# Optimization experiments

Measured on AMD Instinct MI355X. Metric: run time of the kernel, lower is better.

Reference implementation:

```python
import jax, jax.numpy as jnp
import numpy as np

N_HEAD = 16
ROPE_BASE = 10000.0


def _rotate_half(x):
    # interleaved rotate: (-x2, x1) pairs, matching torch stack+flatten
    x1 = x[..., ::2]
    x2 = x[..., 1::2]
    return jnp.stack((-x2, x1), axis=-1).reshape(x.shape)


def setup_inputs() -> dict:
    key = jax.random.key(0)
    ks = jax.random.split(key, 5)
    B, S, C = 4, 2048, 1024
    sc = 1.0 / np.sqrt(C)
    return {
        "x": jax.random.normal(ks[0], (B, S, C), jnp.float32),
        "W_qkv": jax.random.normal(ks[1], (C, 3 * C), jnp.float32) * sc,
        "b_qkv": jax.random.normal(ks[2], (3 * C,), jnp.float32) * 0.02,
        "W_proj": jax.random.normal(ks[3], (C, C), jnp.float32) * sc,
        "b_proj": jax.random.normal(ks[4], (C,), jnp.float32) * 0.02,
    }


def reference(x, W_qkv, b_qkv, W_proj, b_proj):
    B, S, C = x.shape
    H = N_HEAD
    D = C // H

    qkv = x @ W_qkv + b_qkv                       # [B,S,3C]
    q, k, v = jnp.split(qkv, 3, axis=-1)
    q = q.reshape(B, S, H, D).transpose(0, 2, 1, 3)  # [B,H,S,D]
    k = k.reshape(B, S, H, D).transpose(0, 2, 1, 3)
    v = v.reshape(B, S, H, D).transpose(0, 2, 1, 3)

    # RoPE cache (offset=0), faithful to source: emb = cat(freqs, freqs)
    inv_freq = 1.0 / (ROPE_BASE ** (jnp.arange(0, D, 2, dtype=jnp.float32) / D))
    pos = jnp.arange(S, dtype=jnp.float32)
    freqs = jnp.outer(pos, inv_freq)              # [S, D/2]
    emb = jnp.concatenate((freqs, freqs), axis=-1)  # [S, D]
    cos = jnp.cos(emb)[None, None, :, :]
    sin = jnp.sin(emb)[None, None, :, :]

    q = q * cos + _rotate_half(q) * sin
    k = k * cos + _rotate_half(k) * sin

    scale = 1.0 / jnp.sqrt(jnp.asarray(D, x.dtype))
    scores = jnp.einsum("bhqd,bhkd->bhqk", q, k) * scale  # [B,H,S,S]
    causal = jnp.tril(jnp.ones((S, S), dtype=bool))
    scores = jnp.where(causal[None, None], scores, jnp.asarray(-jnp.inf, x.dtype))
    att = jax.nn.softmax(scores, axis=-1)
    out = jnp.einsum("bhqk,bhkd->bhqd", att, v)    # [B,H,S,D]

    out = out.transpose(0, 2, 1, 3).reshape(B, S, C)
    out = out @ W_proj + b_proj                    # dropout=0 (eval)
    return out
```

## Files before the change

### kernel.cpp

```cpp
#include <hip/hip_runtime.h>
#include <hip/hip_bf16.h>
#include <math.h>

#define B_ 4
#define S_ 2048
#define C_ 1024
#define H_ 16
#define D_ 64
#define M_ (B_*S_)
#define NQKV (3*C_)
#define KDIM C_

typedef float f32x4 __attribute__((ext_vector_type(4)));
typedef float f32x16 __attribute__((ext_vector_type(16)));
typedef short bf16x8 __attribute__((ext_vector_type(8)));

static __device__ __forceinline__ ushort f2bf(float f){
    __hip_bfloat16 h = __float2bfloat16(f);
    union { __hip_bfloat16 b; ushort u; } v; v.b = h;
    return v.u;
}

static __device__ __forceinline__ void gload16(const ushort* g, ushort* l){
    __builtin_amdgcn_global_load_lds((__attribute__((address_space(1))) void*)g,
                                     (__attribute__((address_space(3))) void*)l,
                                     16, 0, 0);
}

__global__ void k_conv(const float* __restrict__ in, ushort* __restrict__ out, int n4){
    int i = blockIdx.x*blockDim.x + threadIdx.x;
    if (i < n4){
        float4 v = *(const float4*)(in + i*4);
        ushort4 o;
        o.x = f2bf(v.x); o.y = f2bf(v.y); o.z = f2bf(v.z); o.w = f2bf(v.w);
        *(ushort4*)(out + i*4) = o;
    }
}

__global__ void k_transpose(const float* __restrict__ in, ushort* __restrict__ out,
                            int R, int Ccol){
    __shared__ float tile[32][33];
    int c0 = blockIdx.x*32, r0 = blockIdx.y*32;
    int tx = threadIdx.x, ty = threadIdx.y;
    for (int j = ty; j < 32; j += 8)
        tile[j][tx] = in[(r0 + j)*Ccol + c0 + tx];
    __syncthreads();
    for (int j = ty; j < 32; j += 8)
        out[(size_t)(c0 + tx)*R + r0 + j] = f2bf(tile[j][tx]);
}

__global__ void k_cs_tab(unsigned* __restrict__ csT){
    int t = blockIdx.x*blockDim.x + threadIdx.x;
    if (t >= D_*S_) return;
    int d = t >> 11, pos = t & 2047;
    float invf = powf(10000.0f, -(float)(d & 31) / 32.0f);
    float ang = (float)pos * invf;
    csT[t] = (unsigned)f2bf(cosf(ang)) | ((unsigned)f2bf(sinf(ang)) << 16);
}

__launch_bounds__(512, 4)
__global__ void k_qkv(const ushort* __restrict__ xb, const ushort* __restrict__ wt,
                      const float* __restrict__ bqkv, const unsigned* __restrict__ csT,
                      ushort* __restrict__ qb, ushort* __restrict__ kb, ushort* __restrict__ vT){
    __shared__ __align__(16) ushort As[2][256][32];
    __shared__ __align__(16) ushort Bs[2][128][32];
    int bid = blockIdx.x;
    int lin = (bid & 7)*96 + (bid >> 3);
    int bx = lin % 24, by = lin / 24;
    int M0 = by*256, N0 = bx*128;
    int tid = threadIdx.x;
    int wid = tid >> 6, lane = tid & 63;
    int wm = wid >> 1, wn = wid & 1;
    int lrow = lane & 15, lk = lane >> 4;
    int swu = (lrow >> 1) & 3;

    int scol = (((lane & 3) ^ ((lane >> 3) & 3))) * 8;
    const ushort* gA0 = &xb[(size_t)(M0 + wid*16 + (lane >> 2))*KDIM + scol];
    const ushort* gA1 = gA0 + (size_t)128*KDIM;
    const ushort* gB0 = &wt[(size_t)(N0 + wid*16 + (lane >> 2))*KDIM + scol];

    f32x4 acc[4][4] = {};
    gload16(gA0, &As[0][wid*16][0]);
    gload16(gA1, &As[0][128 + wid*16][0]);
    gload16(gB0, &Bs[0][wid*16][0]);

    int cur = 0;
    for (int k0 = 0; k0 < KDIM; k0 += 32){
        int nk = k0 + 32;
        if (nk < KDIM){
            gload16(gA0 + nk, &As[cur^1][wid*16][0]);
            gload16(gA1 + nk, &As[cur^1][128 + wid*16][0]);
            gload16(gB0 + nk, &Bs[cur^1][wid*16][0]);
            __builtin_amdgcn_sched_barrier(0);
            asm volatile("s_waitcnt vmcnt(3)" ::: "memory");
        } else {
            asm volatile("s_waitcnt vmcnt(0)" ::: "memory");
        }
        __builtin_amdgcn_s_barrier();
        __builtin_amdgcn_sched_barrier(0);
        bf16x8 a[4], b[4];
#pragma unroll
        for (int mi = 0; mi < 4; mi++)
            a[mi] = *(const bf16x8*)(&As[cur][wm*64 + mi*16 + lrow][(lk ^ swu)*8]);
#pragma unroll
        for (int ni = 0; ni < 4; ni++)
            b[ni] = *(const bf16x8*)(&Bs[cur][wn*64 + ni*16 + lrow][(lk ^ swu)*8]);
#pragma unroll
        for (int mi = 0; mi < 4; mi++)
#pragma unroll
            for (int ni = 0; ni < 4; ni++)
                acc[mi][ni] = __builtin_amdgcn_mfma_f32_16x16x32_bf16(a[mi], b[ni], acc[mi][ni], 0, 0, 0);
        __builtin_amdgcn_sched_barrier(0);
        asm volatile("s_waitcnt lgkmcnt(0)" ::: "memory");
        __builtin_amdgcn_s_barrier();
        cur ^= 1;
    }
#pragma unroll
    for (int mi = 0; mi < 4; mi++)
#pragma unroll
    for (int ni = 0; ni < 4; ni++){
        int gn = N0 + wn*64 + ni*16 + lrow;
        float bias = bqkv[gn];
        int which = gn >> 10;
        int cn = gn & 1023;
        int h = cn >> 6, d = cn & 63;
        int gm0 = M0 + wm*64 + mi*16 + lk*4;
        int bb = gm0 >> 11, pos0 = gm0 & 2047;
        if (which == 2){
            ushort4 o = { f2bf(acc[mi][ni][0] + bias), f2bf(acc[mi][ni][1] + bias),
                          f2bf(acc[mi][ni][2] + bias), f2bf(acc[mi][ni][3] + bias) };
            *(ushort4*)(&vT[(((size_t)(bb*H_ + h))*D_ + d)*S_ + pos0]) = o;
        } else {
            uint4 cs4 = *(const uint4*)(&csT[d*2048 + pos0]);
            unsigned csa[4] = { cs4.x, cs4.y, cs4.z, cs4.w };
#pragma unroll
            for (int rr = 0; rr < 4; rr++){
                float val = acc[mi][ni][rr] + bias;
                float rot = __shfl_xor(val, 1);
                unsigned cs = csa[rr];
                float c = __uint_as_float(cs << 16);
                float s = __uint_as_float(cs & 0xffff0000u);
                float o = val*c + ((d & 1) ? rot : -rot)*s;
                if (which == 0) o *= 0.18033688f;
                int out_idx = (((bb*H_ + h)*S_) + pos0 + rr)*D_ + d;
                ((which == 0) ? qb : kb)[out_idx] = f2bf(o);
            }
        }
    }
}

__launch_bounds__(512, 4)
__global__ void k_proj(const ushort* __restrict__ ab, const ushort* __restrict__ wt,
                       const float* __restrict__ bias, float* __restrict__ out){
    __shared__ __align__(16) ushort As[2][256][32];
    __shared__ __align__(16) ushort Bs[2][128][32];
    int bid = blockIdx.x;
    int lin = (bid & 7)*32 + (bid >> 3);
    int bx = lin & 7, by = lin >> 3;
    int M0 = by*256, N0 = bx*128;
    int tid = threadIdx.x;
    int wid = tid >> 6, lane = tid & 63;
    int wm = wid >> 1, wn = wid & 1;
    int lrow = lane & 15, lk = lane >> 4;
    int swu = (lrow >> 1) & 3;

    int scol = (((lane & 3) ^ ((lane >> 3) & 3))) * 8;
    const ushort* gA0 = &ab[(size_t)(M0 + wid*16 + (lane >> 2))*KDIM + scol];
    const ushort* gA1 = gA0 + (size_t)128*KDIM;
    const ushort* gB0 = &wt[(size_t)(N0 + wid*16 + (lane >> 2))*KDIM + scol];

    f32x4 acc[4][4] = {};
    gload16(gA0, &As[0][wid*16][0]);
    gload16(gA1, &As[0][128 + wid*16][0]);
    gload16(gB0, &Bs[0][wid*16][0]);

    int cur = 0;
    for (int k0 = 0; k0 < KDIM; k0 += 32){
        int nk = k0 + 32;
        if (nk < KDIM){
            gload16(gA0 + nk, &As[cur^1][wid*16][0]);
            gload16(gA1 + nk, &As[cur^1][128 + wid*16][0]);
            gload16(gB0 + nk, &Bs[cur^1][wid*16][0]);
            __builtin_amdgcn_sched_barrier(0);
            asm volatile("s_waitcnt vmcnt(3)" ::: "memory");
        } else {
            asm volatile("s_waitcnt vmcnt(0)" ::: "memory");
        }
        __builtin_amdgcn_s_barrier();
        __builtin_amdgcn_sched_barrier(0);
        bf16x8 a[4], b[4];
#pragma unroll
        for (int mi = 0; mi < 4; mi++)
            a[mi] = *(const bf16x8*)(&As[cur][wm*64 + mi*16 + lrow][(lk ^ swu)*8]);
#pragma unroll
        for (int ni = 0; ni < 4; ni++)
            b[ni] = *(const bf16x8*)(&Bs[cur][wn*64 + ni*16 + lrow][(lk ^ swu)*8]);
#pragma unroll
        for (int mi = 0; mi < 4; mi++)
#pragma unroll
            for (int ni = 0; ni < 4; ni++)
                acc[mi][ni] = __builtin_amdgcn_mfma_f32_16x16x32_bf16(a[mi], b[ni], acc[mi][ni], 0, 0, 0);
        __builtin_amdgcn_sched_barrier(0);
        asm volatile("s_waitcnt lgkmcnt(0)" ::: "memory");
        __builtin_amdgcn_s_barrier();
        cur ^= 1;
    }
#pragma unroll
    for (int mi = 0; mi < 4; mi++)
#pragma unroll
    for (int ni = 0; ni < 4; ni++){
        int gn = N0 + wn*64 + ni*16 + lrow;
        float bv = bias[gn];
#pragma unroll
        for (int rr = 0; rr < 4; rr++){
            int gm = M0 + wm*64 + mi*16 + lk*4 + rr;
            out[(size_t)gm*C_ + gn] = acc[mi][ni][rr] + bv;
        }
    }
}

__launch_bounds__(256, 3)
__global__ void k_attn(const ushort* __restrict__ qb, const ushort* __restrict__ kb,
                       const ushort* __restrict__ vT, ushort* __restrict__ ob){
    __shared__ __align__(16) ushort Ks[64][64];
    __shared__ __align__(16) ushort Vs[64][64];
    int bh = blockIdx.x;
    int qt = (gridDim.y - 1) - blockIdx.y;
    int bb = bh >> 4, h = bh & 15;
    int tid = threadIdx.x, wid = tid >> 6, lane = tid & 63;
    int lq = lane & 31, hi = lane >> 5;
    const ushort* qp = qb + (size_t)bh*S_*D_;
    const ushort* kp = kb + (size_t)bh*S_*D_;
    const ushort* vp = vT + (size_t)bh*D_*S_;
    int qw = qt*128 + wid*32;
    int qrow = qw + lq;
    int swz = lq & 7;

    bf16x8 fq[4];
#pragma unroll
    for (int c = 0; c < 4; c++)
        fq[c] = *(const bf16x8*)(&qp[qrow*D_ + c*16 + hi*8]);

    f32x16 acc0 = {}, acc1 = {};
    float m = -1e30f, l = 0.0f;

    int tr = tid >> 3, tcu = tid & 7;
    int twu = (tcu ^ (tr & 7)) * 8;
    int tc = tcu * 8;

    int4 ra = *(const int4*)(&kp[tr*D_ + tc]);
    int4 rb = *(const int4*)(&kp[(tr+32)*D_ + tc]);
    int4 rc = *(const int4*)(&vp[(size_t)tr*S_ + tc]);
    int4 rd = *(const int4*)(&vp[(size_t)(tr+32)*S_ + tc]);

    int nit = 2*qt + 2;
    for (int it = 0; it < nit; ++it){
        int j0 = it*64;
        *(int4*)(&Ks[tr][twu])    = ra;
        *(int4*)(&Ks[tr+32][twu]) = rb;
        *(int4*)(&Vs[tr][twu])    = rc;
        *(int4*)(&Vs[tr+32][twu]) = rd;
        __syncthreads();
        if (it + 1 < nit){
            int j1 = j0 + 64;
            ra = *(const int4*)(&kp[(j1+tr)*D_ + tc]);
            rb = *(const int4*)(&kp[(j1+tr+32)*D_ + tc]);
            rc = *(const int4*)(&vp[(size_t)tr*S_ + j1 + tc]);
            rd = *(const int4*)(&vp[(size_t)(tr+32)*S_ + j1 + tc]);
        }
        int rel = qw - j0;
        if (rel >= 0){
            bool diag0 = (rel == 0);
            bool have1 = (rel >= 32);
            bool diag1 = (rel == 32);
            f32x16 z0 = {}, z1 = {};
#pragma unroll
            for (int c = 0; c < 4; c++){
                bf16x8 kf = *(const bf16x8*)(&Ks[lq][((2*c + hi) ^ swz)*8]);
                z0 = __builtin_amdgcn_mfma_f32_32x32x16_bf16(kf, fq[c], z0, 0, 0, 0);
            }
            if (have1){
#pragma unroll
                for (int c = 0; c < 4; c++){
                    bf16x8 kf = *(const bf16x8*)(&Ks[32 + lq][((2*c + hi) ^ swz)*8]);
                    z1 = __builtin_amdgcn_mfma_f32_32x32x16_bf16(kf, fq[c], z1, 0, 0, 0);
                }
            }
            if (diag0){
#pragma unroll
                for (int r = 0; r < 16; r++)
                    if (((r & 3) + 8*(r >> 2) + 4*hi) > lq) z0[r] = -1e30f;
            }
            if (diag1){
#pragma unroll
                for (int r = 0; r < 16; r++)
                    if (((r & 3) + 8*(r >> 2) + 4*hi) > lq) z1[r] = -1e30f;
            }
            float tmax = z0[0];
#pragma unroll
            for (int r = 1; r < 16; r++) tmax = fmaxf(tmax, z0[r]);
            if (have1){
#pragma unroll
                for (int r = 0; r < 16; r++) tmax = fmaxf(tmax, z1[r]);
            }
            tmax = fmaxf(tmax, __shfl_xor(tmax, 32));
            if (__any(tmax > m)){
                float newm = fmaxf(m, tmax);
                float resc = exp2f(m - newm);
                m = newm; l *= resc;
#pragma unroll
                for (int r = 0; r < 16; r++){ acc0[r] *= resc; acc1[r] *= resc; }
            }
            float rsum = 0.0f;
#pragma unroll
            for (int r = 0; r < 16; r++){ z0[r] = exp2f(z0[r] - m); rsum += z0[r]; }
            if (have1){
#pragma unroll
                for (int r = 0; r < 16; r++){ z1[r] = exp2f(z1[r] - m); rsum += z1[r]; }
            }
            rsum += __shfl_xor(rsum, 32);
            l += rsum;

#define PV_SUB(zz, r0_, su, t) do {                                              \
    unsigned w0, w1, w2, w3;                                                     \
    asm("v_cvt_pk_bf16_f32 %0, %1, %2" : "=v"(w0) : "v"(zz[r0_+0]), "v"(zz[r0_+1])); \
    asm("v_cvt_pk_bf16_f32 %0, %1, %2" : "=v"(w1) : "v"(zz[r0_+2]), "v"(zz[r0_+3])); \
    asm("v_cvt_pk_bf16_f32 %0, %1, %2" : "=v"(w2) : "v"(zz[r0_+4]), "v"(zz[r0_+5])); \
    asm("v_cvt_pk_bf16_f32 %0, %1, %2" : "=v"(w3) : "v"(zz[r0_+6]), "v"(zz[r0_+7])); \
    auto s02 = __builtin_amdgcn_permlane32_swap(w0, w2, false, false);            \
    auto s13 = __builtin_amdgcn_permlane32_swap(w1, w3, false, false);            \
    union { unsigned u[4]; bf16x8 v; } pf;                                       \
    pf.u[0] = s02[0]; pf.u[1] = s13[0]; pf.u[2] = s02[1]; pf.u[3] = s13[1];      \
    bf16x8 vf0 = *(const bf16x8*)(&Vs[lq][(((su)*4 + (t)*2 + hi) ^ swz)*8]);     \
    acc0 = __builtin_amdgcn_mfma_f32_32x32x16_bf16(vf0, pf.v, acc0, 0, 0, 0);    \
    bf16x8 vf1 = *(const bf16x8*)(&Vs[32 + lq][(((su)*4 + (t)*2 + hi) ^ swz)*8]);\
    acc1 = __builtin_amdgcn_mfma_f32_32x32x16_bf16(vf1, pf.v, acc1, 0, 0, 0);    \
} while(0)

            PV_SUB(z0, 0, 0, 0);
            PV_SUB(z0, 8, 0, 1);
            if (have1){
                PV_SUB(z1, 0, 1, 0);
                PV_SUB(z1, 8, 1, 1);
            }
#undef PV_SUB
        }
        __syncthreads();
    }
    float rl = 1.0f / l;
#pragma unroll
    for (int rg = 0; rg < 4; rg++){
        ushort4 o0 = { f2bf(acc0[rg*4+0]*rl), f2bf(acc0[rg*4+1]*rl),
                       f2bf(acc0[rg*4+2]*rl), f2bf(acc0[rg*4+3]*rl) };
        *(ushort4*)(&ob[((size_t)(bb*S_ + qrow))*C_ + h*D_ + rg*8 + hi*4]) = o0;
        ushort4 o1 = { f2bf(acc1[rg*4+0]*rl), f2bf(acc1[rg*4+1]*rl),
                       f2bf(acc1[rg*4+2]*rl), f2bf(acc1[rg*4+3]*rl) };
        *(ushort4*)(&ob[((size_t)(bb*S_ + qrow))*C_ + h*D_ + 32 + rg*8 + hi*4]) = o1;
    }
}

extern "C" void kernel_launch(void* const* d_in, const int* in_sizes, int n_in,
                              void* d_out, int out_size, void* d_ws, size_t ws_size,
                              hipStream_t stream) {
    const float* x     = (const float*)d_in[0];
    const float* Wqkv  = (const float*)d_in[1];
    const float* bqkv  = (const float*)d_in[2];
    const float* Wproj = (const float*)d_in[3];
    const float* bproj = (const float*)d_in[4];
    float* out = (float*)d_out;

    char* ws = (char*)d_ws;
    ushort*   xb   = (ushort*)(ws);
    ushort*   wqt  = (ushort*)(ws + (16u<<20));
    ushort*   wpt  = (ushort*)(ws + (22u<<20));
    unsigned* csT  = (unsigned*)(ws + (24u<<20));
    ushort*   qbuf = (ushort*)(ws + (25u<<20));
    ushort*   kbuf = (ushort*)(ws + (41u<<20));
    ushort*   vbuf = (ushort*)(ws + (57u<<20));
    ushort*   obuf = (ushort*)(ws + (73u<<20));

    k_conv<<<(M_*KDIM/4 + 255)/256, 256, 0, stream>>>(x, xb, M_*KDIM/4);
    dim3 tb(32, 8);
    k_transpose<<<dim3(NQKV/32, KDIM/32), tb, 0, stream>>>(Wqkv, wqt, KDIM, NQKV);
    k_transpose<<<dim3(C_/32, KDIM/32), tb, 0, stream>>>(Wproj, wpt, KDIM, C_);
    k_cs_tab<<<(D_*S_ + 255)/256, 256, 0, stream>>>(csT);

    k_qkv<<<768, 512, 0, stream>>>(xb, wqt, bqkv, csT, qbuf, kbuf, vbuf);
    k_attn<<<dim3(B_*H_, S_/128), 256, 0, stream>>>(qbuf, kbuf, vbuf, obuf);
    k_proj<<<256, 512, 0, stream>>>(obuf, wpt, bproj, out);
}
```

Baseline: 200.7 us.

## Merge prep kernels into one launch, simplify GEMM sync, add attention setprio

Folds the four preprocessing kernels (x bf16 conversion, two weight transposes, RoPE cos/sin table) into one kernel that picks its job by block-index range. This cuts launch count and tail gaps between small kernels. The QKV and projection GEMM loops drop the hand-placed vmcnt/lgkmcnt waits and sched barriers in favour of plain __syncthreads, with one sync after the prologue. That may change how well the next-tile loads overlap with the MFMAs. The attention kernel raises wave priority around the QK and PV MFMA blocks so matrix work is issued ahead of other waves.

```diff
diff --git a/kernel.cpp b/kernel.cpp
--- a/kernel.cpp
+++ b/kernel.cpp
@@ -27,35 +27,44 @@
                                      16, 0, 0);
 }
 
-__global__ void k_conv(const float* __restrict__ in, ushort* __restrict__ out, int n4){
-    int i = blockIdx.x*blockDim.x + threadIdx.x;
-    if (i < n4){
-        float4 v = *(const float4*)(in + i*4);
-        ushort4 o;
-        o.x = f2bf(v.x); o.y = f2bf(v.y); o.z = f2bf(v.z); o.w = f2bf(v.w);
-        *(ushort4*)(out + i*4) = o;
-    }
-}
-
-__global__ void k_transpose(const float* __restrict__ in, ushort* __restrict__ out,
-                            int R, int Ccol){
+__global__ void k_prep(const float* __restrict__ x, const float* __restrict__ Wqkv,
+                       const float* __restrict__ Wproj,
+                       ushort* __restrict__ xb, ushort* __restrict__ wqt,
+                       ushort* __restrict__ wpt, unsigned* __restrict__ csT){
     __shared__ float tile[32][33];
-    int c0 = blockIdx.x*32, r0 = blockIdx.y*32;
-    int tx = threadIdx.x, ty = threadIdx.y;
-    for (int j = ty; j < 32; j += 8)
-        tile[j][tx] = in[(r0 + j)*Ccol + c0 + tx];
-    __syncthreads();
-    for (int j = ty; j < 32; j += 8)
-        out[(size_t)(c0 + tx)*R + r0 + j] = f2bf(tile[j][tx]);
-}
-
-__global__ void k_cs_tab(unsigned* __restrict__ csT){
-    int t = blockIdx.x*blockDim.x + threadIdx.x;
-    if (t >= D_*S_) return;
-    int d = t >> 11, pos = t & 2047;
-    float invf = powf(10000.0f, -(float)(d & 31) / 32.0f);
-    float ang = (float)pos * invf;
-    csT[t] = (unsigned)f2bf(cosf(ang)) | ((unsigned)f2bf(sinf(ang)) << 16);
+    int blk = blockIdx.x, tid = threadIdx.x;
+    if (blk < 2048){
+        const int n4 = M_*KDIM/4;
+        for (int i = blk*256 + tid; i < n4; i += 2048*256){
+            float4 v = *(const float4*)(x + (size_t)i*4);
+            ushort4 o = { f2bf(v.x), f2bf(v.y), f2bf(v.z), f2bf(v.w) };
+            *(ushort4*)(xb + (size_t)i*4) = o;
+        }
+    } else if (blk < 5120){
+        int t = blk - 2048;
+        int c0 = (t % 96)*32, r0 = (t / 96)*32;
+        int tx = tid & 31, ty = tid >> 5;
+        for (int j = ty; j < 32; j += 8)
+            tile[j][tx] = Wqkv[(size_t)(r0 + j)*NQKV + c0 + tx];
+        __syncthreads();
+        for (int j = ty; j < 32; j += 8)
+            wqt[(size_t)(c0 + tx)*KDIM + r0 + j] = f2bf(tile[j][tx]);
+    } else if (blk < 6144){
+        int t = blk - 5120;
+        int c0 = (t & 31)*32, r0 = (t >> 5)*32;
+        int tx = tid & 31, ty = tid >> 5;
+        for (int j = ty; j < 32; j += 8)
+            tile[j][tx] = Wproj[(size_t)(r0 + j)*C_ + c0 + tx];
+        __syncthreads();
+        for (int j = ty; j < 32; j += 8)
+            wpt[(size_t)(c0 + tx)*KDIM + r0 + j] = f2bf(tile[j][tx]);
+    } else {
+        int t = (blk - 6144)*256 + tid;
+        int d = t >> 11, pos = t & 2047;
+        float invf = powf(10000.0f, -(float)(d & 31) / 32.0f);
+        float ang = (float)pos * invf;
+        csT[t] = (unsigned)f2bf(cosf(ang)) | ((unsigned)f2bf(sinf(ang)) << 16);
+    }
 }
 
 __launch_bounds__(512, 4)
@@ -80,24 +89,19 @@
     const ushort* gB0 = &wt[(size_t)(N0 + wid*16 + (lane >> 2))*KDIM + scol];
 
     f32x4 acc[4][4] = {};
+    int cur = 0;
     gload16(gA0, &As[0][wid*16][0]);
     gload16(gA1, &As[0][128 + wid*16][0]);
     gload16(gB0, &Bs[0][wid*16][0]);
-
-    int cur = 0;
+    __syncthreads();
+
     for (int k0 = 0; k0 < KDIM; k0 += 32){
         int nk = k0 + 32;
         if (nk < KDIM){
             gload16(gA0 + nk, &As[cur^1][wid*16][0]);
             gload16(gA1 + nk, &As[cur^1][128 + wid*16][0]);
             gload16(gB0 + nk, &Bs[cur^1][wid*16][0]);
-            __builtin_amdgcn_sched_barrier(0);
-            asm volatile("s_waitcnt vmcnt(3)" ::: "memory");
-        } else {
-            asm volatile("s_waitcnt vmcnt(0)" ::: "memory");
-        }
-        __builtin_amdgcn_s_barrier();
-        __builtin_amdgcn_sched_barrier(0);
+        }
         bf16x8 a[4], b[4];
 #pragma unroll
         for (int mi = 0; mi < 4; mi++)
@@ -110,9 +114,7 @@
 #pragma unroll
             for (int ni = 0; ni < 4; ni++)
                 acc[mi][ni] = __builtin_amdgcn_mfma_f32_16x16x32_bf16(a[mi], b[ni], acc[mi][ni], 0, 0, 0);
-        __builtin_amdgcn_sched_barrier(0);
-        asm volatile("s_waitcnt lgkmcnt(0)" ::: "memory");
-        __builtin_amdgcn_s_barrier();
+        __syncthreads();
         cur ^= 1;
     }
 #pragma unroll
@@ -170,24 +172,19 @@
     const ushort* gB0 = &wt[(size_t)(N0 + wid*16 + (lane >> 2))*KDIM + scol];
 
     f32x4 acc[4][4] = {};
+    int cur = 0;
     gload16(gA0, &As[0][wid*16][0]);
     gload16(gA1, &As[0][128 + wid*16][0]);
     gload16(gB0, &Bs[0][wid*16][0]);
-
-    int cur = 0;
+    __syncthreads();
+
     for (int k0 = 0; k0 < KDIM; k0 += 32){
         int nk = k0 + 32;
         if (nk < KDIM){
             gload16(gA0 + nk, &As[cur^1][wid*16][0]);
             gload16(gA1 + nk, &As[cur^1][128 + wid*16][0]);
             gload16(gB0 + nk, &Bs[cur^1][wid*16][0]);
-            __builtin_amdgcn_sched_barrier(0);
-            asm volatile("s_waitcnt vmcnt(3)" ::: "memory");
-        } else {
-            asm volatile("s_waitcnt vmcnt(0)" ::: "memory");
-        }
-        __builtin_amdgcn_s_barrier();
-        __builtin_amdgcn_sched_barrier(0);
+        }
         bf16x8 a[4], b[4];
 #pragma unroll
         for (int mi = 0; mi < 4; mi++)
@@ -200,9 +197,7 @@
 #pragma unroll
             for (int ni = 0; ni < 4; ni++)
                 acc[mi][ni] = __builtin_amdgcn_mfma_f32_16x16x32_bf16(a[mi], b[ni], acc[mi][ni], 0, 0, 0);
-        __builtin_amdgcn_sched_barrier(0);
-        asm volatile("s_waitcnt lgkmcnt(0)" ::: "memory");
-        __builtin_amdgcn_s_barrier();
+        __syncthreads();
         cur ^= 1;
     }
 #pragma unroll
@@ -274,6 +269,7 @@
             bool have1 = (rel >= 32);
             bool diag1 = (rel == 32);
             f32x16 z0 = {}, z1 = {};
+            __builtin_amdgcn_s_setprio(1);
 #pragma unroll
             for (int c = 0; c < 4; c++){
                 bf16x8 kf = *(const bf16x8*)(&Ks[lq][((2*c + hi) ^ swz)*8]);
@@ -286,6 +282,7 @@
                     z1 = __builtin_amdgcn_mfma_f32_32x32x16_bf16(kf, fq[c], z1, 0, 0, 0);
                 }
             }
+            __builtin_amdgcn_s_setprio(0);
             if (diag0){
 #pragma unroll
                 for (int r = 0; r < 16; r++)
@@ -337,12 +334,14 @@
     acc1 = __builtin_amdgcn_mfma_f32_32x32x16_bf16(vf1, pf.v, acc1, 0, 0, 0);    \
 } while(0)
 
+            __builtin_amdgcn_s_setprio(1);
             PV_SUB(z0, 0, 0, 0);
             PV_SUB(z0, 8, 0, 1);
             if (have1){
                 PV_SUB(z1, 0, 1, 0);
                 PV_SUB(z1, 8, 1, 1);
             }
+            __builtin_amdgcn_s_setprio(0);
 #undef PV_SUB
         }
         __syncthreads();
@@ -379,12 +378,7 @@
     ushort*   vbuf = (ushort*)(ws + (57u<<20));
     ushort*   obuf = (ushort*)(ws + (73u<<20));
 
-    k_conv<<<(M_*KDIM/4 + 255)/256, 256, 0, stream>>>(x, xb, M_*KDIM/4);
-    dim3 tb(32, 8);
-    k_transpose<<<dim3(NQKV/32, KDIM/32), tb, 0, stream>>>(Wqkv, wqt, KDIM, NQKV);
-    k_transpose<<<dim3(C_/32, KDIM/32), tb, 0, stream>>>(Wproj, wpt, KDIM, C_);
-    k_cs_tab<<<(D_*S_ + 255)/256, 256, 0, stream>>>(csT);
-
+    k_prep<<<6656, 256, 0, stream>>>(x, Wqkv, Wproj, xb, wqt, wpt, csT);
     k_qkv<<<768, 512, 0, stream>>>(xb, wqt, bqkv, csT, qbuf, kbuf, vbuf);
     k_attn<<<dim3(B_*H_, S_/128), 256, 0, stream>>>(qbuf, kbuf, vbuf, obuf);
     k_proj<<<256, 512, 0, stream>>>(obuf, wpt, bproj, out);
```

Result: faster. 190.4 us (-5.1%).
